# Optimization experiments

Hardware: AMD Instinct MI355X
Metric: run time of the kernel (lower is better)

## Reference

```python
import jax, jax.numpy as jnp
import numpy as np

K = 1024      # num_embeddings
D = 256       # embedding_dim
BETA = 0.25
DECAY = 0.99
EPS = 1e-05


def setup_inputs() -> dict:
    key = jax.random.key(0)
    k1, k2 = jax.random.split(key)
    z_e = jax.random.normal(k1, (32, D, 32, 32), dtype=jnp.float32)
    embedding = jax.random.normal(k2, (K, D), dtype=jnp.float32)
    ema_cluster_size = jnp.zeros((K,), dtype=jnp.float32)
    ema_w = embedding  # buffer initialized as a clone of the codebook
    return {"z_e": z_e, "embedding": embedding,
            "ema_cluster_size": ema_cluster_size, "ema_w": ema_w}


def reference(z_e, embedding, ema_cluster_size, ema_w):
    B, Dd, H, W = z_e.shape
    # (B, D, H, W) -> (N, D)
    flat_z = jnp.transpose(z_e, (0, 2, 3, 1)).reshape(-1, Dd)

    # L2 distance argmin (||z||^2 + ||e||^2 - 2 z.e)
    dist = (jnp.sum(flat_z * flat_z, axis=1, keepdims=True)
            + jnp.sum(embedding * embedding, axis=1)
            - 2.0 * flat_z @ embedding.T)
    indices = jnp.argmin(dist, axis=1)  # (N,)

    # EMA update (operates on detached values; buffers updated in-place in torch)
    flat_z_sg = jax.lax.stop_gradient(flat_z)
    cluster_size = jax.ops.segment_sum(
        jnp.ones_like(indices, dtype=z_e.dtype), indices, num_segments=K)
    new_ema_cluster_size = DECAY * ema_cluster_size + (1.0 - DECAY) * cluster_size
    dw = jax.ops.segment_sum(flat_z_sg, indices, num_segments=K)  # one_hot.T @ flat_z
    new_ema_w = DECAY * ema_w + (1.0 - DECAY) * dw
    new_embedding = new_ema_w / (new_ema_cluster_size + EPS)[:, None]

    # Gather uses the *updated* codebook (torch copies into the buffer first)
    z_q_flat = new_embedding[indices]                      # (N, D)
    z_q = jnp.transpose(z_q_flat.reshape(B, H, W, Dd), (0, 3, 1, 2))

    # Straight-through estimator + commitment loss
    z_q_st = z_e + jax.lax.stop_gradient(z_q - z_e)
    vq_loss = BETA * jnp.mean((z_e - jax.lax.stop_gradient(z_q)) ** 2)

    return (z_q_st, vq_loss, indices.reshape(B, H, W),
            new_embedding, new_ema_cluster_size, new_ema_w)
```

## Files before the change

kernel.cpp:

```cpp
#include <hip/hip_runtime.h>
#include <stdint.h>

#define N_ROWS 32768
#define K_CODES 1024
#define D_DIM 256
#define NELEM 8388608

#define WS_COUNTS 0
#define WS_LOSS 1030
#define WS_ENORM 263168
#define WS_ROWBEST_BYTES 1056768
#define WS_IDX_BYTES 1318912

#define O_ZQ 0
#define O_LOSS 8388608
#define O_IDX 8388609
#define O_EMB 8421377
#define O_CS 8683521
#define O_EMAW 8684545

#define EP_BYTE_OFF 33685520

typedef _Float16 half8 __attribute__((ext_vector_type(8)));
typedef float f32x16 __attribute__((ext_vector_type(16)));

__device__ __forceinline__ unsigned int fenc(float f) {
    unsigned int u = __float_as_uint(f);
    return (u & 0x80000000u) ? ~u : (u | 0x80000000u);
}
__device__ __forceinline__ unsigned long long umin64(unsigned long long a, unsigned long long b) {
    return a < b ? a : b;
}
__device__ __forceinline__ void gll16(const void* g, void* l) {
    __builtin_amdgcn_global_load_lds((const __attribute__((address_space(1))) void*)g,
                                     (__attribute__((address_space(3))) void*)l, 16, 0, 0);
}

__global__ __launch_bounds__(256) void k_conv_e(const float* __restrict__ emb,
                                                _Float16* __restrict__ Ep,
                                                float* __restrict__ enorm,
                                                float* __restrict__ ws) {
    int k = blockIdx.x, d = threadIdx.x;
    int gid = k * 256 + d;
    if (gid < 2048) ws[gid] = 0.0f;
    unsigned long long* rb = (unsigned long long*)((char*)ws + WS_ROWBEST_BYTES);
    if (gid < N_ROWS) rb[gid] = 0xFFFFFFFFFFFFFFFFull;

    float v = emb[k * 256 + d];
    _Float16 h = (_Float16)v;
    _Float16 l = (_Float16)(v - (float)h);
    int s = d >> 3, sub = d & 7;
    Ep[((size_t)s * 1024 + k) * 8 + sub] = h;
    Ep[((size_t)(32 + s) * 1024 + k) * 8 + sub] = l;
    float sq = v * v;
    #pragma unroll
    for (int off = 32; off >= 1; off >>= 1) sq += __shfl_down(sq, off, 64);
    __shared__ float red[4];
    if ((d & 63) == 0) red[d >> 6] = sq;
    __syncthreads();
    if (d == 0) enorm[k] = (red[0] + red[1]) + (red[2] + red[3]);
}

__global__ __launch_bounds__(256) void k_conv_z(const float* __restrict__ z_e,
                                                _Float16* __restrict__ Zp,
                                                float* __restrict__ lossacc) {
    __shared__ float lt[64 * 68];
    __shared__ float red[4];
    int t = threadIdx.x;
    int hw0 = blockIdx.x * 64, d0 = blockIdx.y * 64, b = blockIdx.z;
    const float* src = z_e + (size_t)b * 262144 + (size_t)d0 * 1024 + hw0;
    int dl = t >> 4, hl = (t & 15) * 4;
    float sq = 0.0f;
    #pragma unroll
    for (int i = 0; i < 4; i++) {
        int d = dl + i * 16;
        float4 v = *(const float4*)(src + (size_t)d * 1024 + hl);
        sq += v.x * v.x + v.y * v.y + v.z * v.z + v.w * v.w;
        lt[(hl + 0) * 68 + d] = v.x;
        lt[(hl + 1) * 68 + d] = v.y;
        lt[(hl + 2) * 68 + d] = v.z;
        lt[(hl + 3) * 68 + d] = v.w;
    }
    __syncthreads();
    int hr = t >> 2, seg = t & 3;
    int n = b * 1024 + hw0 + hr;
    int sg0 = (d0 >> 3) + seg * 2;
    half8 hi[2], lo[2];
    #pragma unroll
    for (int p = 0; p < 2; p++) {
        #pragma unroll
        for (int j = 0; j < 8; j++) {
            float v = lt[hr * 68 + seg * 16 + p * 8 + j];
            _Float16 h = (_Float16)v;
            hi[p][j] = h;
            lo[p][j] = (_Float16)(v - (float)h);
        }
    }
    *(half8*)(Zp + ((size_t)(sg0 + 0) * 32768 + n) * 8) = hi[0];
    *(half8*)(Zp + ((size_t)(sg0 + 1) * 32768 + n) * 8) = hi[1];
    *(half8*)(Zp + ((size_t)(32 + sg0) * 32768 + n) * 8) = lo[0];
    *(half8*)(Zp + ((size_t)(33 + sg0) * 32768 + n) * 8) = lo[1];
    #pragma unroll
    for (int off = 32; off >= 1; off >>= 1) sq += __shfl_down(sq, off, 64);
    if ((t & 63) == 0) red[t >> 6] = sq;
    __syncthreads();
    if (t == 0) atomicAdd(lossacc, (red[0] + red[1]) + (red[2] + red[3]));
}

__global__ __launch_bounds__(256, 4) void k_mm(const _Float16* __restrict__ Zp,
                                               const _Float16* __restrict__ Ep,
                                               const float* __restrict__ enorm,
                                               unsigned long long* __restrict__ row_best) {
    __shared__ __align__(16) char smem[32768];

    int t = threadIdx.x;
    int lane = t & 63, wv = t >> 6;
    int b = blockIdx.x;
    int wgid = (b & 7) * 256 + (b >> 3);
    int rt = wgid >> 3;
    int ct = wgid & 7;
    int row0 = rt * 128, code0 = ct * 128;

    int wr = wv >> 1, wc = wv & 1;
    int m31 = lane & 31, ko = lane >> 5;

    f32x16 acc[2][2];
    #pragma unroll
    for (int m = 0; m < 2; m++)
        #pragma unroll
        for (int n = 0; n < 2; n++)
            #pragma unroll
            for (int r = 0; r < 16; r++) acc[m][n][r] = 0.0f;

    int quad = wv;
    bool isZ = quad < 2;
    int lobias = (quad & 1) ? 32 : 0;
    size_t gstride = isZ ? (size_t)32768 * 16 : (size_t)1024 * 16;
    const char* gsel = isZ
        ? (const char*)Zp + ((size_t)row0 + lane) * 16
        : (const char*)Ep + ((size_t)code0 + lane) * 16;
    char* lbase = smem + quad * 4096;

    auto STAGE = [&](int g, int buf) {
        #pragma unroll
        for (int s = 0; s < 2; s++) {
            const char* src = gsel + (size_t)(lobias + 2 * g + s) * gstride;
            char* dst = lbase + buf * 16384 + s * 2048;
            gll16(src, dst);
            gll16(src + 64 * 16, dst + 64 * 16);
        }
    };

    STAGE(0, 0);
    STAGE(1, 1);
    asm volatile("s_waitcnt vmcnt(4)" ::: "memory");
    __builtin_amdgcn_s_barrier();
    asm volatile("" ::: "memory");

    for (int g = 0; g < 16; g++) {
        const _Float16* zh = (const _Float16*)(smem + (g & 1) * 16384);
        const _Float16* zl = zh + 2048;
        const _Float16* eh = zh + 4096;
        const _Float16* el = zh + 6144;
        __builtin_amdgcn_s_setprio(1);
        {
            half8 azh[2], azl[2], beh[2], bel[2];
            #pragma unroll
            for (int i = 0; i < 2; i++) {
                azh[i] = *(const half8*)(zh + (ko * 128 + wr * 64 + 32 * i + m31) * 8);
                azl[i] = *(const half8*)(zl + (ko * 128 + wr * 64 + 32 * i + m31) * 8);
                beh[i] = *(const half8*)(eh + (ko * 128 + wc * 64 + 32 * i + m31) * 8);
                bel[i] = *(const half8*)(el + (ko * 128 + wc * 64 + 32 * i + m31) * 8);
            }
            #pragma unroll
            for (int i = 0; i < 2; i++)
                #pragma unroll
                for (int j = 0; j < 2; j++) {
                    acc[i][j] = __builtin_amdgcn_mfma_f32_32x32x16_f16(azh[i], beh[j], acc[i][j], 0, 0, 0);
                    acc[i][j] = __builtin_amdgcn_mfma_f32_32x32x16_f16(azl[i], beh[j], acc[i][j], 0, 0, 0);
                    acc[i][j] = __builtin_amdgcn_mfma_f32_32x32x16_f16(azh[i], bel[j], acc[i][j], 0, 0, 0);
                }
        }
        __builtin_amdgcn_s_setprio(0);
        asm volatile("s_waitcnt lgkmcnt(0)" ::: "memory");
        __builtin_amdgcn_s_barrier();
        if (g < 14) STAGE(g + 2, g & 1);
        if (g < 15) {
            if (g < 14) asm volatile("s_waitcnt vmcnt(4)" ::: "memory");
            else        asm volatile("s_waitcnt vmcnt(0)" ::: "memory");
            __builtin_amdgcn_s_barrier();
            asm volatile("" ::: "memory");
        }
    }

    unsigned long long* slot = (unsigned long long*)smem;
    float en0 = enorm[code0 + wc * 64 + m31];
    float en1 = enorm[code0 + wc * 64 + 32 + m31];
    unsigned int col0 = code0 + wc * 64 + m31;
    unsigned int col1 = col0 + 32;

    if (wc == 0) {
        #pragma unroll
        for (int m = 0; m < 2; m++)
            #pragma unroll
            for (int j = 0; j < 16; j++) {
                int row = wr * 64 + m * 32 + 4 * ko + (j & 3) + 8 * (j >> 2);
                unsigned long long p0 = ((unsigned long long)fenc(en0 - 2.0f * acc[m][0][j]) << 32) | col0;
                unsigned long long p1 = ((unsigned long long)fenc(en1 - 2.0f * acc[m][1][j]) << 32) | col1;
                slot[row * 32 + ((m31 + row) & 31)] = umin64(p0, p1);
            }
    }
    __syncthreads();
    if (wc != 0) {
        #pragma unroll
        for (int m = 0; m < 2; m++)
            #pragma unroll
            for (int j = 0; j < 16; j++) {
                int row = wr * 64 + m * 32 + 4 * ko + (j & 3) + 8 * (j >> 2);
                unsigned long long p0 = ((unsigned long long)fenc(en0 - 2.0f * acc[m][0][j]) << 32) | col0;
                unsigned long long p1 = ((unsigned long long)fenc(en1 - 2.0f * acc[m][1][j]) << 32) | col1;
                atomicMin(&slot[row * 32 + ((m31 + row) & 31)], umin64(p0, p1));
            }
    }
    __syncthreads();
    if (t < 128) {
        unsigned long long mm = slot[t * 32 + (t & 31)];
        #pragma unroll
        for (int i = 1; i < 32; i++) mm = umin64(mm, slot[t * 32 + ((i + t) & 31)]);
        atomicMin(&row_best[row0 + t], mm);
    }
}

__global__ __launch_bounds__(256) void k_fin_idx(const unsigned long long* __restrict__ rb,
                                                 int* __restrict__ idxs,
                                                 float* __restrict__ counts,
                                                 float* __restrict__ out) {
    __shared__ float hist[K_CODES];
    int t = threadIdx.x;
    #pragma unroll
    for (int j = 0; j < 4; j++) hist[j * 256 + t] = 0.0f;
    __syncthreads();
    int i = blockIdx.x * 256 + t;
    int id = (int)(rb[i] & 0xFFFFFFFFull);
    idxs[i] = id;
    out[O_IDX + i] = (float)id;
    atomicAdd(&hist[id], 1.0f);
    __syncthreads();
    #pragma unroll
    for (int j = 0; j < 4; j++) {
        float h = hist[j * 256 + t];
        if (h != 0.0f) atomicAdd(&counts[j * 256 + t], h);
    }
}

__global__ __launch_bounds__(512) void k_dw(const float* __restrict__ z_e,
                                            const int* __restrict__ idxs,
                                            float* __restrict__ dw) {
    __shared__ float acc[2 * K_CODES];
    int t = threadIdx.x;
    int d = blockIdx.x;
    #pragma unroll
    for (int j = 0; j < 4; j++) acc[j * 512 + t] = 0.0f;
    __syncthreads();
    int rep = (t & 1) * K_CODES;
    for (int b = 0; b < 32; b++) {
        int2 id2 = *(const int2*)(idxs + b * 1024 + t * 2);
        float2 v = *(const float2*)(z_e + (size_t)b * 262144 + (size_t)d * 1024 + t * 2);
        atomicAdd(&acc[rep + id2.x], v.x);
        atomicAdd(&acc[rep + id2.y], v.y);
    }
    __syncthreads();
    float* pr = dw + (size_t)d * 1024;
    #pragma unroll
    for (int j = 0; j < 2; j++) pr[j * 512 + t] = acc[j * 512 + t] + acc[K_CODES + j * 512 + t];
}

__global__ __launch_bounds__(256) void k_red(const float* __restrict__ dw,
                                             const float* __restrict__ ema_cs,
                                             const float* __restrict__ ema_w,
                                             const float* __restrict__ counts,
                                             float* __restrict__ lossacc,
                                             float* __restrict__ out) {
    __shared__ float tile[64 * 69];
    __shared__ float csl[64];
    __shared__ float craw[64];
    __shared__ float red[4];
    int t = threadIdx.x;
    int k0 = blockIdx.x * 64, d0 = blockIdx.y * 64;
    int dr = t >> 4, kc = t & 15;
    if (t < 64) {
        float c = counts[k0 + t];
        craw[t] = c;
        csl[t] = 0.99f * ema_cs[k0 + t] + 0.01f * c;
    }
    #pragma unroll
    for (int q = 0; q < 4; q++) {
        float4 v = *(const float4*)(dw + (size_t)(d0 + dr + 16 * q) * 1024 + k0 + kc * 4);
        float* p = tile + (dr + 16 * q) * 69 + kc * 4;
        p[0] = v.x; p[1] = v.y; p[2] = v.z; p[3] = v.w;
    }
    __syncthreads();
    int kk = t >> 2, dq = t & 3;
    int k = k0 + kk;
    float inv = 1.0f / (csl[kk] + 1e-5f);
    float cr = craw[kk];
    float lterm = 0.0f;
    #pragma unroll
    for (int j4 = 0; j4 < 4; j4++) {
        int dd = dq * 16 + j4 * 4;
        size_t kd = (size_t)k * 256 + d0 + dd;
        float4 w = *(const float4*)(ema_w + kd);
        float s0 = tile[(dd + 0) * 69 + kk];
        float s1 = tile[(dd + 1) * 69 + kk];
        float s2 = tile[(dd + 2) * 69 + kk];
        float s3 = tile[(dd + 3) * 69 + kk];
        float4 nw;
        nw.x = 0.99f * w.x + 0.01f * s0;
        nw.y = 0.99f * w.y + 0.01f * s1;
        nw.z = 0.99f * w.z + 0.01f * s2;
        nw.w = 0.99f * w.w + 0.01f * s3;
        *(float4*)(out + O_EMAW + kd) = nw;
        float4 ne = {nw.x * inv, nw.y * inv, nw.z * inv, nw.w * inv};
        *(float4*)(out + O_EMB + kd) = ne;
        lterm += ne.x * (cr * ne.x - 2.0f * s0);
        lterm += ne.y * (cr * ne.y - 2.0f * s1);
        lterm += ne.z * (cr * ne.z - 2.0f * s2);
        lterm += ne.w * (cr * ne.w - 2.0f * s3);
    }
    if (blockIdx.y == 0 && t < 64) out[O_CS + k0 + t] = csl[t];
    #pragma unroll
    for (int off = 32; off >= 1; off >>= 1) lterm += __shfl_down(lterm, off, 64);
    if ((t & 63) == 0) red[t >> 6] = lterm;
    __syncthreads();
    if (t == 0) atomicAdd(lossacc, (red[0] + red[1]) + (red[2] + red[3]));
}

__global__ __launch_bounds__(256) void k_bcast(const int* __restrict__ idxs,
                                               const float* __restrict__ lossacc,
                                               float* __restrict__ out) {
    __shared__ float lt[64 * 68];
    __shared__ int sid[64];
    int t = threadIdx.x;
    int hw0 = blockIdx.x * 64, d0 = blockIdx.y * 64, b = blockIdx.z;
    if (t < 64) sid[t] = idxs[b * 1024 + hw0 + t];
    __syncthreads();
    int r = t >> 2, c = t & 3;
    const float* nrow = out + O_EMB + (size_t)sid[r] * 256 + d0;
    #pragma unroll
    for (int it = 0; it < 4; it++) {
        int dd = it * 16 + c * 4;
        float4 q = *(const float4*)(nrow + dd);
        float* p = lt + r * 68 + dd;
        p[0] = q.x; p[1] = q.y; p[2] = q.z; p[3] = q.w;
    }
    __syncthreads();
    int dl = t >> 4, hl = (t & 15) * 4;
    float* dst = out + O_ZQ + (size_t)b * 262144 + (size_t)d0 * 1024 + hw0;
    #pragma unroll
    for (int i = 0; i < 4; i++) {
        int d = dl + i * 16;
        float4 w;
        w.x = lt[(hl + 0) * 68 + d];
        w.y = lt[(hl + 1) * 68 + d];
        w.z = lt[(hl + 2) * 68 + d];
        w.w = lt[(hl + 3) * 68 + d];
        *(float4*)(dst + (size_t)d * 1024 + hl) = w;
    }
    if (blockIdx.x == 0 && blockIdx.y == 0 && blockIdx.z == 0 && t == 0)
        out[O_LOSS] = lossacc[0] * 2.9802322387695312e-08f;
}

extern "C" void kernel_launch(void* const* d_in, const int* in_sizes, int n_in,
                              void* d_out, int out_size, void* d_ws, size_t ws_size,
                              hipStream_t stream) {
    const float* z_e = (const float*)d_in[0];
    const float* emb = (const float*)d_in[1];
    const float* ema_cs = (const float*)d_in[2];
    const float* ema_w = (const float*)d_in[3];
    float* out = (float*)d_out;
    float* ws = (float*)d_ws;

    float* counts = ws + WS_COUNTS;
    float* lossacc = ws + WS_LOSS;
    float* enorm = ws + WS_ENORM;
    unsigned long long* row_best = (unsigned long long*)((char*)d_ws + WS_ROWBEST_BYTES);
    int* idxs = (int*)((char*)d_ws + WS_IDX_BYTES);

    _Float16* Zp = (_Float16*)d_out;
    _Float16* Ep = (_Float16*)((char*)d_out + EP_BYTE_OFF);
    float* dw = (float*)d_out;

    k_conv_e<<<1024, 256, 0, stream>>>(emb, Ep, enorm, ws);
    k_conv_z<<<dim3(16, 4, 32), 256, 0, stream>>>(z_e, Zp, lossacc);
    k_mm<<<2048, 256, 0, stream>>>(Zp, Ep, enorm, row_best);
    k_fin_idx<<<128, 256, 0, stream>>>(row_best, idxs, counts, out);
    k_dw<<<256, 512, 0, stream>>>(z_e, idxs, dw);
    k_red<<<dim3(16, 4), 256, 0, stream>>>(dw, ema_cs, ema_w, counts, lossacc, out);
    k_bcast<<<dim3(16, 4, 32), 256, 0, stream>>>(idxs, lossacc, out);
}
```

Baseline: 232.9 us.

## Merge conversion kernels, fold index finalization into matmul tail, shrink indices

```diff
diff --git a/kernel.cpp b/kernel.cpp
--- a/kernel.cpp
+++ b/kernel.cpp
@@ -11,6 +11,7 @@
 #define WS_ENORM 263168
 #define WS_ROWBEST_BYTES 1056768
 #define WS_IDX_BYTES 1318912
+#define WS_RTDONE_BYTES 1384448
 
 #define O_ZQ 0
 #define O_LOSS 8388608
@@ -36,46 +37,48 @@
                                      (__attribute__((address_space(3))) void*)l, 16, 0, 0);
 }
 
-__global__ __launch_bounds__(256) void k_conv_e(const float* __restrict__ emb,
-                                                _Float16* __restrict__ Ep,
-                                                float* __restrict__ enorm,
-                                                float* __restrict__ ws) {
-    int k = blockIdx.x, d = threadIdx.x;
-    int gid = k * 256 + d;
-    if (gid < 2048) ws[gid] = 0.0f;
-    unsigned long long* rb = (unsigned long long*)((char*)ws + WS_ROWBEST_BYTES);
-    if (gid < N_ROWS) rb[gid] = 0xFFFFFFFFFFFFFFFFull;
-
-    float v = emb[k * 256 + d];
-    _Float16 h = (_Float16)v;
-    _Float16 l = (_Float16)(v - (float)h);
-    int s = d >> 3, sub = d & 7;
-    Ep[((size_t)s * 1024 + k) * 8 + sub] = h;
-    Ep[((size_t)(32 + s) * 1024 + k) * 8 + sub] = l;
-    float sq = v * v;
-    #pragma unroll
-    for (int off = 32; off >= 1; off >>= 1) sq += __shfl_down(sq, off, 64);
-    __shared__ float red[4];
-    if ((d & 63) == 0) red[d >> 6] = sq;
-    __syncthreads();
-    if (d == 0) enorm[k] = (red[0] + red[1]) + (red[2] + red[3]);
-}
-
-__global__ __launch_bounds__(256) void k_conv_z(const float* __restrict__ z_e,
-                                                _Float16* __restrict__ Zp,
-                                                float* __restrict__ lossacc) {
+__global__ __launch_bounds__(256) void k_conv(const float* __restrict__ z_e,
+                                              const float* __restrict__ emb,
+                                              _Float16* __restrict__ Zp,
+                                              _Float16* __restrict__ Ep,
+                                              float* __restrict__ enorm,
+                                              float* __restrict__ ws) {
     __shared__ float lt[64 * 68];
     __shared__ float red[4];
     int t = threadIdx.x;
-    int hw0 = blockIdx.x * 64, d0 = blockIdx.y * 64, b = blockIdx.z;
+    int gid = blockIdx.x;
+
+    if (gid >= 2048) {
+        int k = gid - 2048, d = t;
+        int g2 = k * 256 + d;
+        if (g2 < 2048) ws[g2] = 0.0f;
+        unsigned long long* rb = (unsigned long long*)((char*)ws + WS_ROWBEST_BYTES);
+        if (g2 < N_ROWS) rb[g2] = 0xFFFFFFFFFFFFFFFFull;
+        int* rtd = (int*)((char*)ws + WS_RTDONE_BYTES);
+        if (g2 < 256) rtd[g2] = 0;
+
+        float v = emb[k * 256 + d];
+        _Float16 h = (_Float16)v;
+        _Float16 l = (_Float16)(v - (float)h);
+        int s = d >> 3, sub = d & 7;
+        Ep[((size_t)s * 1024 + k) * 8 + sub] = h;
+        Ep[((size_t)(32 + s) * 1024 + k) * 8 + sub] = l;
+        float sq = v * v;
+        #pragma unroll
+        for (int off = 32; off >= 1; off >>= 1) sq += __shfl_down(sq, off, 64);
+        if ((d & 63) == 0) red[d >> 6] = sq;
+        __syncthreads();
+        if (d == 0) enorm[k] = (red[0] + red[1]) + (red[2] + red[3]);
+        return;
+    }
+
+    int hw0 = (gid & 15) * 64, d0 = ((gid >> 4) & 3) * 64, b = gid >> 6;
     const float* src = z_e + (size_t)b * 262144 + (size_t)d0 * 1024 + hw0;
     int dl = t >> 4, hl = (t & 15) * 4;
-    float sq = 0.0f;
     #pragma unroll
     for (int i = 0; i < 4; i++) {
         int d = dl + i * 16;
         float4 v = *(const float4*)(src + (size_t)d * 1024 + hl);
-        sq += v.x * v.x + v.y * v.y + v.z * v.z + v.w * v.w;
         lt[(hl + 0) * 68 + d] = v.x;
         lt[(hl + 1) * 68 + d] = v.y;
         lt[(hl + 2) * 68 + d] = v.z;
@@ -100,18 +103,18 @@
     *(half8*)(Zp + ((size_t)(sg0 + 1) * 32768 + n) * 8) = hi[1];
     *(half8*)(Zp + ((size_t)(32 + sg0) * 32768 + n) * 8) = lo[0];
     *(half8*)(Zp + ((size_t)(33 + sg0) * 32768 + n) * 8) = lo[1];
-    #pragma unroll
-    for (int off = 32; off >= 1; off >>= 1) sq += __shfl_down(sq, off, 64);
-    if ((t & 63) == 0) red[t >> 6] = sq;
-    __syncthreads();
-    if (t == 0) atomicAdd(lossacc, (red[0] + red[1]) + (red[2] + red[3]));
 }
 
 __global__ __launch_bounds__(256, 4) void k_mm(const _Float16* __restrict__ Zp,
                                                const _Float16* __restrict__ Ep,
                                                const float* __restrict__ enorm,
-                                               unsigned long long* __restrict__ row_best) {
+                                               unsigned long long* __restrict__ row_best,
+                                               unsigned short* __restrict__ idxs,
+                                               float* __restrict__ counts,
+                                               int* __restrict__ rt_done,
+                                               float* __restrict__ out) {
     __shared__ __align__(16) char smem[32768];
+    __shared__ int islast;
 
     int t = threadIdx.x;
     int lane = t & 63, wv = t >> 6;
@@ -229,43 +232,52 @@
         for (int i = 1; i < 32; i++) mm = umin64(mm, slot[t * 32 + ((i + t) & 31)]);
         atomicMin(&row_best[row0 + t], mm);
     }
-}
-
-__global__ __launch_bounds__(256) void k_fin_idx(const unsigned long long* __restrict__ rb,
-                                                 int* __restrict__ idxs,
-                                                 float* __restrict__ counts,
-                                                 float* __restrict__ out) {
-    __shared__ float hist[K_CODES];
-    int t = threadIdx.x;
-    #pragma unroll
-    for (int j = 0; j < 4; j++) hist[j * 256 + t] = 0.0f;
-    __syncthreads();
-    int i = blockIdx.x * 256 + t;
-    int id = (int)(rb[i] & 0xFFFFFFFFull);
-    idxs[i] = id;
-    out[O_IDX + i] = (float)id;
-    atomicAdd(&hist[id], 1.0f);
-    __syncthreads();
-    #pragma unroll
-    for (int j = 0; j < 4; j++) {
-        float h = hist[j * 256 + t];
-        if (h != 0.0f) atomicAdd(&counts[j * 256 + t], h);
+
+    __syncthreads();
+    if (t == 0) {
+        __threadfence();
+        islast = (atomicAdd(&rt_done[rt], 1) == 7);
+    }
+    __syncthreads();
+    if (islast) {
+        __threadfence();
+        float* hist = (float*)smem;
+        #pragma unroll
+        for (int j = 0; j < 4; j++) hist[j * 256 + t] = 0.0f;
+        __syncthreads();
+        if (t < 128) {
+            unsigned long long v = atomicMin(&row_best[row0 + t], 0xFFFFFFFFFFFFFFFFull);
+            int id = (int)(v & 0xFFFFFFFFull);
+            idxs[row0 + t] = (unsigned short)id;
+            out[O_IDX + row0 + t] = (float)id;
+            atomicAdd(&hist[id], 1.0f);
+        }
+        __syncthreads();
+        #pragma unroll
+        for (int j = 0; j < 4; j++) {
+            float h = hist[j * 256 + t];
+            if (h != 0.0f) atomicAdd(&counts[j * 256 + t], h);
+        }
     }
 }
 
 __global__ __launch_bounds__(512) void k_dw(const float* __restrict__ z_e,
-                                            const int* __restrict__ idxs,
-                                            float* __restrict__ dw) {
+                                            const unsigned short* __restrict__ idxs,
+                                            float* __restrict__ dw,
+                                            float* __restrict__ lossacc) {
     __shared__ float acc[2 * K_CODES];
+    __shared__ float red8[8];
     int t = threadIdx.x;
     int d = blockIdx.x;
     #pragma unroll
     for (int j = 0; j < 4; j++) acc[j * 512 + t] = 0.0f;
     __syncthreads();
     int rep = (t & 1) * K_CODES;
+    float sq = 0.0f;
     for (int b = 0; b < 32; b++) {
-        int2 id2 = *(const int2*)(idxs + b * 1024 + t * 2);
+        ushort2 id2 = *(const ushort2*)(idxs + b * 1024 + t * 2);
         float2 v = *(const float2*)(z_e + (size_t)b * 262144 + (size_t)d * 1024 + t * 2);
+        sq += v.x * v.x + v.y * v.y;
         atomicAdd(&acc[rep + id2.x], v.x);
         atomicAdd(&acc[rep + id2.y], v.y);
     }
@@ -273,6 +285,16 @@
     float* pr = dw + (size_t)d * 1024;
     #pragma unroll
     for (int j = 0; j < 2; j++) pr[j * 512 + t] = acc[j * 512 + t] + acc[K_CODES + j * 512 + t];
+    #pragma unroll
+    for (int off = 32; off >= 1; off >>= 1) sq += __shfl_down(sq, off, 64);
+    if ((t & 63) == 0) red8[t >> 6] = sq;
+    __syncthreads();
+    if (t == 0) {
+        float s = 0.0f;
+        #pragma unroll
+        for (int j = 0; j < 8; j++) s += red8[j];
+        atomicAdd(lossacc, s);
+    }
 }
 
 __global__ __launch_bounds__(256) void k_red(const float* __restrict__ dw,
@@ -335,7 +357,7 @@
     if (t == 0) atomicAdd(lossacc, (red[0] + red[1]) + (red[2] + red[3]));
 }
 
-__global__ __launch_bounds__(256) void k_bcast(const int* __restrict__ idxs,
+__global__ __launch_bounds__(256) void k_bcast(const unsigned short* __restrict__ idxs,
                                                const float* __restrict__ lossacc,
                                                float* __restrict__ out) {
     __shared__ float lt[64 * 68];
@@ -384,17 +406,16 @@
     float* lossacc = ws + WS_LOSS;
     float* enorm = ws + WS_ENORM;
     unsigned long long* row_best = (unsigned long long*)((char*)d_ws + WS_ROWBEST_BYTES);
-    int* idxs = (int*)((char*)d_ws + WS_IDX_BYTES);
+    unsigned short* idxs = (unsigned short*)((char*)d_ws + WS_IDX_BYTES);
+    int* rt_done = (int*)((char*)d_ws + WS_RTDONE_BYTES);
 
     _Float16* Zp = (_Float16*)d_out;
     _Float16* Ep = (_Float16*)((char*)d_out + EP_BYTE_OFF);
     float* dw = (float*)d_out;
 
-    k_conv_e<<<1024, 256, 0, stream>>>(emb, Ep, enorm, ws);
-    k_conv_z<<<dim3(16, 4, 32), 256, 0, stream>>>(z_e, Zp, lossacc);
-    k_mm<<<2048, 256, 0, stream>>>(Zp, Ep, enorm, row_best);
-    k_fin_idx<<<128, 256, 0, stream>>>(row_best, idxs, counts, out);
-    k_dw<<<256, 512, 0, stream>>>(z_e, idxs, dw);
+    k_conv<<<3072, 256, 0, stream>>>(z_e, emb, Zp, Ep, enorm, ws);
+    k_mm<<<2048, 256, 0, stream>>>(Zp, Ep, enorm, row_best, idxs, counts, rt_done, out);
+    k_dw<<<256, 512, 0, stream>>>(z_e, idxs, dw, lossacc);
     k_red<<<dim3(16, 4), 256, 0, stream>>>(dw, ema_cs, ema_w, counts, lossacc, out);
     k_bcast<<<dim3(16, 4, 32), 256, 0, stream>>>(idxs, lossacc, out);
 }
```

Measured after the change: 261.7 us. 1.12x slower.
